# Performance work log

Measured on AMD Instinct MI355X. Metric: run time of the kernel, lower is better.

Reference implementation:

```python
import jax, jax.numpy as jnp
import numpy as np

SCALE = 0.08838834764831845  # 1/sqrt(head_dim=128)


def setup_inputs() -> dict:
    key = jax.random.key(0)
    ks = jax.random.split(key, 5)
    B, H, D = 16, 8, 128          # batch (decode seqs), kv heads, head_dim
    BS, BPS = 16, 128             # block_size, blocks per sequence
    NBLK = B * BPS                # total cache blocks (2048)
    CTX = 2048                    # context length per sequence
    q = jax.random.normal(ks[0], (B, H, D), jnp.float32)
    k = jax.random.normal(ks[1], (B, H, D), jnp.float32)
    v = jax.random.normal(ks[2], (B, H, D), jnp.float32)
    k_cache = jax.random.normal(ks[3], (NBLK, BS, H, D), jnp.float32)
    v_cache = jax.random.normal(ks[4], (NBLK, BS, H, D), jnp.float32)
    # each sequence owns a distinct contiguous set of blocks
    block_tables = jnp.arange(B * BPS, dtype=jnp.int32).reshape(B, BPS)
    context_lens = jnp.full((B,), CTX, dtype=jnp.int32)
    # slot for the newest token (position CTX-1) of each sequence
    last = CTX - 1
    slot_mapping = block_tables[:, last // BS] * BS + (last % BS)
    return {"q": q, "k": k, "v": v, "k_cache": k_cache, "v_cache": v_cache,
            "slot_mapping": slot_mapping.astype(jnp.int32),
            "block_tables": block_tables, "context_lens": context_lens}


def reference(q, k, v, k_cache, v_cache, slot_mapping, block_tables, context_lens):
    # ---- store_kvcache: scatter new k/v tokens into paged caches ----
    nblk, bs, H, D = k_cache.shape
    k_cache = k_cache.reshape(nblk * bs, H, D).at[slot_mapping].set(k).reshape(nblk, bs, H, D)
    v_cache = v_cache.reshape(nblk * bs, H, D).at[slot_mapping].set(v).reshape(nblk, bs, H, D)

    # ---- _sdpa_decode: paged gather + masked attention (q_per_seq = 1) ----
    B, nb = block_tables.shape
    T = nb * bs                              # max tokens per sequence
    token_idx = jnp.arange(T, dtype=jnp.int32)
    block_idx = token_idx // bs
    token_off = token_idx % bs
    block_ids = block_tables[:, block_idx]   # [B, T]
    k_all = k_cache[block_ids, token_off]    # [B, T, H, D]
    v_all = v_cache[block_ids, token_off]    # [B, T, H, D]

    valid = token_idx[None, :] < context_lens[:, None]           # [B, T]
    q_pos = context_lens - 1                                     # q_per_seq == 1
    causal = token_idx[None, :] <= q_pos[:, None]                # [B, T]
    mask = valid & causal

    scores = jnp.einsum("bhd,bthd->bht", q, k_all) * SCALE       # [B, H, T]
    scores = jnp.where(mask[:, None, :], scores, -jnp.inf)
    p = jax.nn.softmax(scores, axis=-1)
    out = jnp.einsum("bht,bthd->bhd", p, v_all)                  # [B, H, D]
    return out
```

## Files before the change

### kernel.cpp

```cpp
#include <hip/hip_runtime.h>
#include <math.h>

#define B_ 16
#define H_ 8
#define D_ 128
#define BS_ 16
#define BPS_ 128
#define T_ (BPS_ * BS_)
#define NSPLIT 16
#define CHUNK (T_ / NSPLIT)
#define NBLK_C (CHUNK / BS_)
#define SCALE_ 0.08838834764831845f

__global__ __launch_bounds__(256, 8) void attn_partial(
    const float* __restrict__ q,
    const float* __restrict__ knew,
    const float* __restrict__ vnew,
    const float* __restrict__ kc,
    const float* __restrict__ vc,
    const int* __restrict__ btab,
    const int* __restrict__ clen,
    float* __restrict__ ws_m,
    float* __restrict__ ws_l,
    float* __restrict__ ws_o)
{
    const int c = blockIdx.x;
    const int h = blockIdx.y;
    const int b = blockIdx.z;
    const int tid = threadIdx.x;
    const int wave = tid >> 6;
    const int lane = tid & 63;
    const int hl = lane & 31;
    const int half = lane >> 5;
    const int ctx = clen[b];
    const int cs = c * CHUNK;

    __shared__ int   s_bt[NBLK_C];
    __shared__ float s_p[CHUNK];
    __shared__ float s_red[8];
    __shared__ float s_ml[2];
    __shared__ float s_o[8][D_];

    if (tid < NBLK_C) s_bt[tid] = btab[b * BPS_ + c * NBLK_C + tid];

    const float4 q4 = *(const float4*)(q + (size_t)(b * H_ + h) * D_ + 4 * hl);
    __syncthreads();

    #pragma unroll
    for (int o = 0; o < 4; ++o) {
        float4 k4[4];
        int tls[4];
        #pragma unroll
        for (int j = 0; j < 4; ++j) {
            const int tl = wave * 32 + o * 8 + j * 2 + half;
            tls[j] = tl;
            const int tg = cs + tl;
            const int blk = s_bt[tl >> 4];
            const float* kp = (tg == ctx - 1)
                ? (knew + (size_t)(b * H_ + h) * D_)
                : (kc + (((size_t)blk * BS_ + (tg & 15)) * H_ + h) * D_);
            k4[j] = *(const float4*)(kp + 4 * hl);
        }
        #pragma unroll
        for (int j = 0; j < 4; ++j) {
            float s = q4.x * k4[j].x + q4.y * k4[j].y + q4.z * k4[j].z + q4.w * k4[j].w;
            s += __shfl_xor(s, 16);
            s += __shfl_xor(s, 8);
            s += __shfl_xor(s, 4);
            s += __shfl_xor(s, 2);
            s += __shfl_xor(s, 1);
            if (hl == 0) s_p[tls[j]] = (cs + tls[j] < ctx) ? s * SCALE_ : -INFINITY;
        }
    }
    __syncthreads();

    float sc = 0.f;
    if (tid < CHUNK) {
        sc = s_p[tid];
        float m = sc;
        m = fmaxf(m, __shfl_xor(m, 32));
        m = fmaxf(m, __shfl_xor(m, 16));
        m = fmaxf(m, __shfl_xor(m, 8));
        m = fmaxf(m, __shfl_xor(m, 4));
        m = fmaxf(m, __shfl_xor(m, 2));
        m = fmaxf(m, __shfl_xor(m, 1));
        if (lane == 0) s_red[wave] = m;
    }
    __syncthreads();
    if (tid == 0) s_ml[0] = fmaxf(fmaxf(s_red[0], s_red[1]), -1e30f);
    __syncthreads();
    const float m_c = s_ml[0];

    if (tid < CHUNK) {
        const float p = __expf(sc - m_c);
        s_p[tid] = p;
        float l = p;
        l += __shfl_xor(l, 32);
        l += __shfl_xor(l, 16);
        l += __shfl_xor(l, 8);
        l += __shfl_xor(l, 4);
        l += __shfl_xor(l, 2);
        l += __shfl_xor(l, 1);
        if (lane == 0) s_red[4 + wave] = l;
    }
    __syncthreads();
    if (tid == 0) s_ml[1] = s_red[4] + s_red[5];
    __syncthreads();

    float4 acc = make_float4(0.f, 0.f, 0.f, 0.f);
    #pragma unroll
    for (int o = 0; o < 4; ++o) {
        float4 v4[4];
        float pw[4];
        #pragma unroll
        for (int j = 0; j < 4; ++j) {
            const int tl = wave * 32 + o * 8 + j * 2 + half;
            const int tg = cs + tl;
            const int blk = s_bt[tl >> 4];
            const float* vp = (tg == ctx - 1)
                ? (vnew + (size_t)(b * H_ + h) * D_)
                : (vc + (((size_t)blk * BS_ + (tg & 15)) * H_ + h) * D_);
            v4[j] = *(const float4*)(vp + 4 * hl);
            pw[j] = s_p[tl];
        }
        #pragma unroll
        for (int j = 0; j < 4; ++j) {
            acc.x += pw[j] * v4[j].x;
            acc.y += pw[j] * v4[j].y;
            acc.z += pw[j] * v4[j].z;
            acc.w += pw[j] * v4[j].w;
        }
    }
    *(float4*)(&s_o[(wave << 1) | half][4 * hl]) = acc;
    __syncthreads();

    const int idx = (b * H_ + h) * NSPLIT + c;
    if (tid < D_) {
        float oo = 0.f;
        #pragma unroll
        for (int r = 0; r < 8; ++r) oo += s_o[r][tid];
        ws_o[(size_t)idx * D_ + tid] = oo;
    }
    if (tid == 0) {
        ws_m[idx] = s_ml[0];
        ws_l[idx] = s_ml[1];
    }
}

__global__ __launch_bounds__(128) void attn_reduce(
    const float* __restrict__ ws_m,
    const float* __restrict__ ws_l,
    const float* __restrict__ ws_o,
    float* __restrict__ out)
{
    const int bh = blockIdx.x;
    const int d = threadIdx.x;

    float mm[NSPLIT];
    float m_g = -INFINITY;
    #pragma unroll
    for (int c = 0; c < NSPLIT; ++c) {
        mm[c] = ws_m[bh * NSPLIT + c];
        m_g = fmaxf(m_g, mm[c]);
    }
    float l_g = 0.f, acc = 0.f;
    #pragma unroll
    for (int c = 0; c < NSPLIT; ++c) {
        const float co = __expf(mm[c] - m_g);
        l_g += ws_l[bh * NSPLIT + c] * co;
        acc += ws_o[(size_t)(bh * NSPLIT + c) * D_ + d] * co;
    }
    out[(size_t)bh * D_ + d] = acc / l_g;
}

extern "C" void kernel_launch(void* const* d_in, const int* in_sizes, int n_in,
                              void* d_out, int out_size, void* d_ws, size_t ws_size,
                              hipStream_t stream) {
    const float* q    = (const float*)d_in[0];
    const float* knew = (const float*)d_in[1];
    const float* vnew = (const float*)d_in[2];
    const float* kc   = (const float*)d_in[3];
    const float* vc   = (const float*)d_in[4];
    const int* btab = (const int*)d_in[6];
    const int* clen = (const int*)d_in[7];
    float* out = (float*)d_out;

    float* ws   = (float*)d_ws;
    float* ws_m = ws;
    float* ws_l = ws + B_ * H_ * NSPLIT;
    float* ws_o = ws + 2 * B_ * H_ * NSPLIT;

    dim3 grid1(NSPLIT, H_, B_);
    attn_partial<<<grid1, 256, 0, stream>>>(q, knew, vnew, kc, vc, btab, clen,
                                            ws_m, ws_l, ws_o);
    attn_reduce<<<dim3(B_ * H_), D_, 0, stream>>>(ws_m, ws_l, ws_o, out);
}
```

Before: 309.1 us.

## Process all heads per block over contiguous cache rows, raise split count

Each block now handles all 8 heads of one sequence for a context chunk, so every token's full contiguous H*D row (4 KB) is read with coalesced float4 loads instead of scattered 512-byte per-head slices. The number of context splits is templated and picked at runtime from workspace size (64, 32, or 16), giving a grid of NS x B blocks. The reduce kernel is generalized to arbitrary NS with shared-memory coefficients. The cost is larger shared memory per block (16 KB for partial outputs plus scores), more registers for four q/acc vectors, and a larger partial-result workspace.

```diff
diff --git a/kernel.cpp b/kernel.cpp
--- a/kernel.cpp
+++ b/kernel.cpp
@@ -7,12 +7,11 @@
 #define BS_ 16
 #define BPS_ 128
 #define T_ (BPS_ * BS_)
-#define NSPLIT 16
-#define CHUNK (T_ / NSPLIT)
-#define NBLK_C (CHUNK / BS_)
+#define ROW_ (H_ * D_)
 #define SCALE_ 0.08838834764831845f
 
-__global__ __launch_bounds__(256, 8) void attn_partial(
+template<int NS>
+__global__ __launch_bounds__(256) void attn_partial(
     const float* __restrict__ q,
     const float* __restrict__ knew,
     const float* __restrict__ vnew,
@@ -24,9 +23,12 @@
     float* __restrict__ ws_l,
     float* __restrict__ ws_o)
 {
+    constexpr int CHUNK = T_ / NS;
+    constexpr int TPW = CHUNK / 4;
+    constexpr int NBLK_C = CHUNK / BS_;
+
     const int c = blockIdx.x;
-    const int h = blockIdx.y;
-    const int b = blockIdx.z;
+    const int b = blockIdx.y;
     const int tid = threadIdx.x;
     const int wave = tid >> 6;
     const int lane = tid & 63;
@@ -36,117 +38,130 @@
     const int cs = c * CHUNK;
 
     __shared__ int   s_bt[NBLK_C];
-    __shared__ float s_p[CHUNK];
-    __shared__ float s_red[8];
-    __shared__ float s_ml[2];
-    __shared__ float s_o[8][D_];
+    __shared__ float s_p[H_][CHUNK];
+    __shared__ float s_mx[H_], s_l[H_];
+    __shared__ float s_o[4][H_][D_];
 
     if (tid < NBLK_C) s_bt[tid] = btab[b * BPS_ + c * NBLK_C + tid];
 
-    const float4 q4 = *(const float4*)(q + (size_t)(b * H_ + h) * D_ + 4 * hl);
-    __syncthreads();
-
+    float4 q4[4];
     #pragma unroll
-    for (int o = 0; o < 4; ++o) {
-        float4 k4[4];
-        int tls[4];
-        #pragma unroll
-        for (int j = 0; j < 4; ++j) {
-            const int tl = wave * 32 + o * 8 + j * 2 + half;
-            tls[j] = tl;
-            const int tg = cs + tl;
-            const int blk = s_bt[tl >> 4];
-            const float* kp = (tg == ctx - 1)
-                ? (knew + (size_t)(b * H_ + h) * D_)
-                : (kc + (((size_t)blk * BS_ + (tg & 15)) * H_ + h) * D_);
-            k4[j] = *(const float4*)(kp + 4 * hl);
-        }
-        #pragma unroll
-        for (int j = 0; j < 4; ++j) {
-            float s = q4.x * k4[j].x + q4.y * k4[j].y + q4.z * k4[j].z + q4.w * k4[j].w;
-            s += __shfl_xor(s, 16);
-            s += __shfl_xor(s, 8);
-            s += __shfl_xor(s, 4);
-            s += __shfl_xor(s, 2);
-            s += __shfl_xor(s, 1);
-            if (hl == 0) s_p[tls[j]] = (cs + tls[j] < ctx) ? s * SCALE_ : -INFINITY;
-        }
-    }
-    __syncthreads();
-
-    float sc = 0.f;
-    if (tid < CHUNK) {
-        sc = s_p[tid];
-        float m = sc;
-        m = fmaxf(m, __shfl_xor(m, 32));
+    for (int j = 0; j < 4; ++j)
+        q4[j] = *(const float4*)(q + (size_t)b * ROW_ + j * 256 + half * 128 + 4 * hl);
+    __syncthreads();
+
+    #pragma unroll 4
+    for (int i = 0; i < TPW; i += 2) {
+        float4 k4[8];
+        #pragma unroll
+        for (int u = 0; u < 2; ++u) {
+            const int t = wave * TPW + i + u;
+            const int tg = cs + t;
+            const int blk = s_bt[t >> 4];
+            const float* rb = (tg == ctx - 1)
+                ? (knew + (size_t)b * ROW_)
+                : (kc + ((size_t)blk * BS_ + (tg & 15)) * ROW_);
+            #pragma unroll
+            for (int j = 0; j < 4; ++j)
+                k4[u * 4 + j] = *(const float4*)(rb + j * 256 + half * 128 + 4 * hl);
+        }
+        #pragma unroll
+        for (int u = 0; u < 2; ++u) {
+            const int t = wave * TPW + i + u;
+            const int tg = cs + t;
+            #pragma unroll
+            for (int j = 0; j < 4; ++j) {
+                const float4 kv = k4[u * 4 + j];
+                float s = q4[j].x * kv.x + q4[j].y * kv.y + q4[j].z * kv.z + q4[j].w * kv.w;
+                s += __shfl_xor(s, 16);
+                s += __shfl_xor(s, 8);
+                s += __shfl_xor(s, 4);
+                s += __shfl_xor(s, 2);
+                s += __shfl_xor(s, 1);
+                if (hl == 0) s_p[2 * j + half][t] = (tg < ctx) ? s * SCALE_ : -INFINITY;
+            }
+        }
+    }
+    __syncthreads();
+
+    {
+        const int h = tid >> 5;
+        float m = -INFINITY;
+        for (int t = hl; t < CHUNK; t += 32) m = fmaxf(m, s_p[h][t]);
         m = fmaxf(m, __shfl_xor(m, 16));
         m = fmaxf(m, __shfl_xor(m, 8));
         m = fmaxf(m, __shfl_xor(m, 4));
         m = fmaxf(m, __shfl_xor(m, 2));
         m = fmaxf(m, __shfl_xor(m, 1));
-        if (lane == 0) s_red[wave] = m;
-    }
-    __syncthreads();
-    if (tid == 0) s_ml[0] = fmaxf(fmaxf(s_red[0], s_red[1]), -1e30f);
-    __syncthreads();
-    const float m_c = s_ml[0];
-
-    if (tid < CHUNK) {
-        const float p = __expf(sc - m_c);
-        s_p[tid] = p;
-        float l = p;
-        l += __shfl_xor(l, 32);
+        if (hl == 0) s_mx[h] = fmaxf(m, -1e30f);
+    }
+    __syncthreads();
+    {
+        const int h = tid >> 5;
+        const float mx = s_mx[h];
+        float l = 0.f;
+        for (int t = hl; t < CHUNK; t += 32) {
+            const float p = __expf(s_p[h][t] - mx);
+            s_p[h][t] = p;
+            l += p;
+        }
         l += __shfl_xor(l, 16);
         l += __shfl_xor(l, 8);
         l += __shfl_xor(l, 4);
         l += __shfl_xor(l, 2);
         l += __shfl_xor(l, 1);
-        if (lane == 0) s_red[4 + wave] = l;
-    }
-    __syncthreads();
-    if (tid == 0) s_ml[1] = s_red[4] + s_red[5];
-    __syncthreads();
-
-    float4 acc = make_float4(0.f, 0.f, 0.f, 0.f);
+        if (hl == 0) s_l[h] = l;
+    }
+    __syncthreads();
+
+    float4 acc[4];
     #pragma unroll
-    for (int o = 0; o < 4; ++o) {
-        float4 v4[4];
-        float pw[4];
-        #pragma unroll
-        for (int j = 0; j < 4; ++j) {
-            const int tl = wave * 32 + o * 8 + j * 2 + half;
-            const int tg = cs + tl;
-            const int blk = s_bt[tl >> 4];
-            const float* vp = (tg == ctx - 1)
-                ? (vnew + (size_t)(b * H_ + h) * D_)
-                : (vc + (((size_t)blk * BS_ + (tg & 15)) * H_ + h) * D_);
-            v4[j] = *(const float4*)(vp + 4 * hl);
-            pw[j] = s_p[tl];
-        }
-        #pragma unroll
-        for (int j = 0; j < 4; ++j) {
-            acc.x += pw[j] * v4[j].x;
-            acc.y += pw[j] * v4[j].y;
-            acc.z += pw[j] * v4[j].z;
-            acc.w += pw[j] * v4[j].w;
-        }
-    }
-    *(float4*)(&s_o[(wave << 1) | half][4 * hl]) = acc;
-    __syncthreads();
-
-    const int idx = (b * H_ + h) * NSPLIT + c;
-    if (tid < D_) {
-        float oo = 0.f;
-        #pragma unroll
-        for (int r = 0; r < 8; ++r) oo += s_o[r][tid];
-        ws_o[(size_t)idx * D_ + tid] = oo;
-    }
-    if (tid == 0) {
-        ws_m[idx] = s_ml[0];
-        ws_l[idx] = s_ml[1];
-    }
-}
-
+    for (int j = 0; j < 4; ++j) acc[j] = make_float4(0.f, 0.f, 0.f, 0.f);
+    #pragma unroll 4
+    for (int i = 0; i < TPW; i += 2) {
+        float4 v4[8];
+        #pragma unroll
+        for (int u = 0; u < 2; ++u) {
+            const int t = wave * TPW + i + u;
+            const int tg = cs + t;
+            const int blk = s_bt[t >> 4];
+            const float* rb = (tg == ctx - 1)
+                ? (vnew + (size_t)b * ROW_)
+                : (vc + ((size_t)blk * BS_ + (tg & 15)) * ROW_);
+            #pragma unroll
+            for (int j = 0; j < 4; ++j)
+                v4[u * 4 + j] = *(const float4*)(rb + j * 256 + half * 128 + 4 * hl);
+        }
+        #pragma unroll
+        for (int u = 0; u < 2; ++u) {
+            const int t = wave * TPW + i + u;
+            #pragma unroll
+            for (int j = 0; j < 4; ++j) {
+                const float pw = s_p[2 * j + half][t];
+                acc[j].x += pw * v4[u * 4 + j].x;
+                acc[j].y += pw * v4[u * 4 + j].y;
+                acc[j].z += pw * v4[u * 4 + j].z;
+                acc[j].w += pw * v4[u * 4 + j].w;
+            }
+        }
+    }
+    #pragma unroll
+    for (int j = 0; j < 4; ++j)
+        *(float4*)&s_o[wave][2 * j + half][4 * hl] = acc[j];
+    __syncthreads();
+
+    for (int r = tid; r < H_ * D_; r += 256) {
+        const int h = r >> 7, d = r & 127;
+        const float oo = s_o[0][h][d] + s_o[1][h][d] + s_o[2][h][d] + s_o[3][h][d];
+        ws_o[((size_t)(b * H_ + h) * NS + c) * D_ + d] = oo;
+    }
+    if (tid < H_) {
+        ws_m[(b * H_ + tid) * NS + c] = s_mx[tid];
+        ws_l[(b * H_ + tid) * NS + c] = s_l[tid];
+    }
+}
+
+template<int NS>
 __global__ __launch_bounds__(128) void attn_reduce(
     const float* __restrict__ ws_m,
     const float* __restrict__ ws_l,
@@ -154,23 +169,55 @@
     float* __restrict__ out)
 {
     const int bh = blockIdx.x;
-    const int d = threadIdx.x;
-
-    float mm[NSPLIT];
-    float m_g = -INFINITY;
-    #pragma unroll
-    for (int c = 0; c < NSPLIT; ++c) {
-        mm[c] = ws_m[bh * NSPLIT + c];
-        m_g = fmaxf(m_g, mm[c]);
-    }
-    float l_g = 0.f, acc = 0.f;
-    #pragma unroll
-    for (int c = 0; c < NSPLIT; ++c) {
-        const float co = __expf(mm[c] - m_g);
-        l_g += ws_l[bh * NSPLIT + c] * co;
-        acc += ws_o[(size_t)(bh * NSPLIT + c) * D_ + d] * co;
-    }
-    out[(size_t)bh * D_ + d] = acc / l_g;
+    const int tid = threadIdx.x;
+
+    __shared__ float s_co[NS];
+    __shared__ float s_lg;
+
+    if (tid < 64) {
+        float m = -INFINITY;
+        for (int cc = tid; cc < NS; cc += 64) m = fmaxf(m, ws_m[bh * NS + cc]);
+        m = fmaxf(m, __shfl_xor(m, 32));
+        m = fmaxf(m, __shfl_xor(m, 16));
+        m = fmaxf(m, __shfl_xor(m, 8));
+        m = fmaxf(m, __shfl_xor(m, 4));
+        m = fmaxf(m, __shfl_xor(m, 2));
+        m = fmaxf(m, __shfl_xor(m, 1));
+        float lw = 0.f;
+        for (int cc = tid; cc < NS; cc += 64) {
+            const float co = __expf(ws_m[bh * NS + cc] - m);
+            s_co[cc] = co;
+            lw += ws_l[bh * NS + cc] * co;
+        }
+        lw += __shfl_xor(lw, 32);
+        lw += __shfl_xor(lw, 16);
+        lw += __shfl_xor(lw, 8);
+        lw += __shfl_xor(lw, 4);
+        lw += __shfl_xor(lw, 2);
+        lw += __shfl_xor(lw, 1);
+        if (tid == 0) s_lg = lw;
+    }
+    __syncthreads();
+
+    float acc = 0.f;
+    #pragma unroll 8
+    for (int cc = 0; cc < NS; ++cc)
+        acc += s_co[cc] * ws_o[((size_t)bh * NS + cc) * D_ + tid];
+    out[(size_t)bh * D_ + tid] = acc / s_lg;
+}
+
+template<int NS>
+static void launch_all(const float* q, const float* knew, const float* vnew,
+                       const float* kc, const float* vc,
+                       const int* btab, const int* clen,
+                       float* ws, float* out, hipStream_t stream)
+{
+    float* ws_m = ws;
+    float* ws_l = ws + B_ * H_ * NS;
+    float* ws_o = ws + 2 * B_ * H_ * NS;
+    attn_partial<NS><<<dim3(NS, B_), 256, 0, stream>>>(q, knew, vnew, kc, vc,
+                                                       btab, clen, ws_m, ws_l, ws_o);
+    attn_reduce<NS><<<dim3(B_ * H_), 128, 0, stream>>>(ws_m, ws_l, ws_o, out);
 }
 
 extern "C" void kernel_launch(void* const* d_in, const int* in_sizes, int n_in,
@@ -184,14 +231,11 @@
     const int* btab = (const int*)d_in[6];
     const int* clen = (const int*)d_in[7];
     float* out = (float*)d_out;
-
-    float* ws   = (float*)d_ws;
-    float* ws_m = ws;
-    float* ws_l = ws + B_ * H_ * NSPLIT;
-    float* ws_o = ws + 2 * B_ * H_ * NSPLIT;
-
-    dim3 grid1(NSPLIT, H_, B_);
-    attn_partial<<<grid1, 256, 0, stream>>>(q, knew, vnew, kc, vc, btab, clen,
-                                            ws_m, ws_l, ws_o);
-    attn_reduce<<<dim3(B_ * H_), D_, 0, stream>>>(ws_m, ws_l, ws_o, out);
-}
+    float* ws  = (float*)d_ws;
+
+    const size_t need64 = (size_t)B_ * H_ * 64 * (2 + D_) * sizeof(float);
+    const size_t need32 = (size_t)B_ * H_ * 32 * (2 + D_) * sizeof(float);
+    if (ws_size >= need64)      launch_all<64>(q, knew, vnew, kc, vc, btab, clen, ws, out, stream);
+    else if (ws_size >= need32) launch_all<32>(q, knew, vnew, kc, vc, btab, clen, ws, out, stream);
+    else                        launch_all<16>(q, knew, vnew, kc, vc, btab, clen, ws, out, stream);
+}
```

After: 292.5 us. 5.4% less time.
